# Performance work log

Hardware: AMD Instinct MI355X
Metric: run time of the kernel (lower is better)

Reference implementation:

```python
import jax, jax.numpy as jnp
import numpy as np

L, S, R, NUM_RESNET = 6, 2, 3, 3
N = 2 ** L            # 64 blocks per axis
NX = N * S            # 128 grid points per axis
NCART_SIDE = 80
NCART = NCART_SIDE ** 2


def _perm_idx(L_, l):
    delta = 2 ** (L_ - l - 1)
    t = np.tile(np.arange(2) * delta, delta) + np.repeat(np.arange(delta), 2)
    t = np.tile(t, 2 ** l) + np.repeat(np.arange(2 ** l) * 2 ** (L_ - l), 2 ** (L_ - l))
    return jnp.asarray(t)


def _switch_idx(L_):
    h = L_ // 2
    t = np.tile(np.arange(2 ** h) * 2 ** h, 2 ** h) + np.repeat(np.arange(2 ** h), 2 ** h)
    return jnp.asarray(t)


def _bmm2(x, g_left, g_right):
    # x: (B,p,i,q,j). Right block-diag GEMM on (q,j), then left block-diag GEMM on (p,i).
    y = jnp.einsum('bpiqj,qjk->bpiqk', x, g_right)
    return jnp.einsum('bpiqk,pio->bpoqk', y, g_left)


def _complex_layer(xr, xi, p):
    # p: stacked (r1,i1,r2,i2,r3,i3,r4,i4); complex-style cross products of the original.
    r1, i1, r2, i2, r3, i3, r4, i4 = p
    yr = _bmm2(xr, r1, r1) + _bmm2(xr, i1, i1) + _bmm2(xi, r2, i2) + _bmm2(xi, i2, r2)
    yi = _bmm2(xi, r3, r3) + _bmm2(xi, i3, i3) + _bmm2(xr, r4, i4) + _bmm2(xr, i4, r4)
    return yr, yi


def _u_layer(xr, xi, p):
    ur1, ui1, ur2, ui2, ur3, ui3, ur4, ui4 = p
    return (_bmm2(xr, ur1, ur1) + _bmm2(xr, ui2, ui2)
            + _bmm2(xi, ur3, ui3) + _bmm2(xi, ui4, ur4))


def _permute(yr, yi, idx):
    yr = jnp.take(jnp.take(yr, idx, axis=1), idx, axis=3)
    yi = jnp.take(jnp.take(yi, idx, axis=1), idx, axis=3)
    return yr, yi


def _merge(y):  # (B,N,R,N,R) -> (B,N/2,2R,N/2,2R)
    return y.reshape(y.shape[0], N // 2, 2 * R, N // 2, 2 * R)


def _split(y):  # inverse of _merge
    return y.reshape(y.shape[0], N, R, N, R)


def reference(x, Vp, Hp, Mp, Gp, Up, cart_mat, r_index):
    B = x.shape[0]
    xr = x[..., 0].reshape(B, N, S, N, S)
    xi = x[..., 1].reshape(B, N, S, N, S)
    yr, yi = _complex_layer(xr, xi, Vp)                       # (B,N,R,N,R)
    for li, l in enumerate(range(L - 1, L // 2 - 1, -1)):     # H stages (permute then merge-GEMM)
        yr, yi = _permute(yr, yi, _perm_idx(L, l))
        yr, yi = _complex_layer(_merge(yr), _merge(yi), Hp[li])
        yr, yi = _split(yr), _split(yi)
    yr, yi = _permute(yr, yi, _switch_idx(L))                 # middle switch shuffle
    for k in range(NUM_RESNET):                               # residual M blocks
        zr, zi = _complex_layer(yr, yi, Mp[k])
        yr, yi = yr + zr, yi + zi
    for li, l in enumerate(range(L // 2 - 1, -1, -1)):        # G stages (merge-GEMM then permute)
        yr, yi = _complex_layer(_merge(yr), _merge(yi), Gp[li])
        yr, yi = _split(yr), _split(yi)
        yr, yi = _permute(yr, yi, _perm_idx(L, l))
    y = _u_layer(yr, yi, Up).reshape(B, NX * NX)              # real output, (B,NX,NX) flattened
    y = jnp.take(y, r_index, axis=1)                          # polar reindexing
    out = y @ cart_mat.T                                      # polar -> cartesian interpolation
    return out.reshape(B, NCART_SIDE, NCART_SIDE)


def setup_inputs() -> dict:
    key = jax.random.key(0)
    ks = jax.random.split(key, 9)
    B = 128
    x = jax.random.normal(ks[0], (B, NX, NX, 2), dtype=jnp.float32)
    Vp = jax.random.normal(ks[1], (8, N, S, R), dtype=jnp.float32) * 0.35
    Hp = jax.random.normal(ks[2], (L // 2, 8, N // 2, 2 * R, 2 * R), dtype=jnp.float32) * 0.2
    Mp = jax.random.normal(ks[3], (NUM_RESNET, 8, N, R, R), dtype=jnp.float32) * 0.25
    Gp = jax.random.normal(ks[4], (L // 2, 8, N // 2, 2 * R, 2 * R), dtype=jnp.float32) * 0.2
    Up = jax.random.normal(ks[5], (8, N, R, S), dtype=jnp.float32) * 0.35
    cart_mat = jax.random.normal(ks[6], (NCART, NX * NX), dtype=jnp.float32) * 0.01
    r_index = jax.random.permutation(ks[7], NX * NX).astype(jnp.int32)
    return {"x": x, "Vp": Vp, "Hp": Hp, "Mp": Mp, "Gp": Gp, "Up": Up,
            "cart_mat": cart_mat, "r_index": r_index}
```

## Files before the change

kernel.cpp:

```cpp
#include <hip/hip_runtime.h>


typedef __attribute__((ext_vector_type(8))) short sx8;
typedef __attribute__((ext_vector_type(4))) float fx4;
typedef __attribute__((ext_vector_type(8))) unsigned short usx8;
typedef __attribute__((ext_vector_type(4))) unsigned short usx4;

__device__ __forceinline__ unsigned short f2bf(float f) {
  unsigned u = __builtin_bit_cast(unsigned, f);
  u = (u + 0x7FFFu + ((u >> 16) & 1u)) >> 16;
  return (unsigned short)u;
}

template<int ID>
__device__ __forceinline__ int rp_apply(int k) {
  if constexpr (ID == 0) { return k; }
  else if constexpr (ID == 3) { return (k & 7) * 8 + (k >> 3); }
  else {
    constexpr int l = (ID == 1) ? 4 : (ID == 2) ? 3 : (ID == 4) ? 2 : (ID == 5) ? 1 : 0;
    constexpr int d = 1 << (5 - l);
    constexpr int m2 = 2 * d;
    int g = k / m2, r = k % m2;
    return g * m2 + (r & 1) * d + (r >> 1);
  }
}

__global__ __launch_bounds__(256) void k_transpose(const float* __restrict__ x,
                                                   float* __restrict__ xtr,
                                                   float* __restrict__ xti) {
  __shared__ float ls[2][32][129];
  const int t = threadIdx.x;
  const int u = blockIdx.x;
  const int v0 = blockIdx.y * 32;
  for (int it = 0; it < 32; ++it) {
    int b = it * 4 + (t >> 6);
    int r = t & 63;
    int v = r >> 1, ch = r & 1;
    ls[ch][v][b] = x[(((size_t)b * 128 + u) * 128 + (v0 + v)) * 2 + ch];
  }
  __syncthreads();
  for (int it = 0; it < 32; ++it) {
    int idx = it * 256 + t;
    int ch = idx >> 12;
    int v = (idx >> 7) & 31;
    int b = idx & 127;
    float* dst = ch ? xti : xtr;
    dst[((size_t)(u * 128 + v0 + v)) * 128 + b] = ls[ch][v][b];
  }
}

__global__ __launch_bounds__(128) void k_v(const float* __restrict__ xtr,
                                           const float* __restrict__ xti,
                                           float* __restrict__ yr,
                                           float* __restrict__ yi,
                                           const float* __restrict__ wp) {
  const int b = threadIdx.x;
  const int p = blockIdx.x, q = blockIdx.y;
  float X[4], Yr[9], Yi[9];
#pragma unroll
  for (int k = 0; k < 9; ++k) { Yr[k] = 0.f; Yi[k] = 0.f; }

  auto loadX = [&](const float* src) {
#pragma unroll
    for (int i = 0; i < 2; ++i)
#pragma unroll
      for (int j = 0; j < 2; ++j)
        X[i * 2 + j] = src[((size_t)((2 * p + i) * 128 + (2 * q + j))) * 128 + b];
  };
  auto term = [&](float* Y, int lm, int rm) {
    const float* Lw = wp + ((size_t)lm * 64 + p) * 6;
    const float* Rw = wp + ((size_t)rm * 64 + q) * 6;
#pragma unroll
    for (int i = 0; i < 2; ++i) {
      float t0 = X[i*2+0] * Rw[0] + X[i*2+1] * Rw[3];
      float t1 = X[i*2+0] * Rw[1] + X[i*2+1] * Rw[4];
      float t2 = X[i*2+0] * Rw[2] + X[i*2+1] * Rw[5];
#pragma unroll
      for (int o = 0; o < 3; ++o) {
        float lv = Lw[i * 3 + o];
        Y[o*3+0] += lv * t0; Y[o*3+1] += lv * t1; Y[o*3+2] += lv * t2;
      }
    }
  };
  loadX(xtr);
  term(Yr, 0, 0); term(Yr, 1, 1); term(Yi, 6, 7); term(Yi, 7, 6);
  loadX(xti);
  term(Yr, 2, 3); term(Yr, 3, 2); term(Yi, 4, 4); term(Yi, 5, 5);
#pragma unroll
  for (int o = 0; o < 3; ++o)
#pragma unroll
    for (int k = 0; k < 3; ++k) {
      size_t off = ((size_t)((p * 3 + o) * 192 + (q * 3 + k))) * 128 + b;
      yr[off] = Yr[o * 3 + k];
      yi[off] = Yi[o * 3 + k];
    }
}

template<int PERM>
__global__ __launch_bounds__(128) void k_hg(const float* __restrict__ xr,
                                            const float* __restrict__ xi,
                                            float* __restrict__ yr,
                                            float* __restrict__ yi,
                                            const float* __restrict__ wp) {
  const int b = threadIdx.x;
  const int P = blockIdx.x, Q = blockIdx.y;
  int rrow[6], rcol[6];
#pragma unroll
  for (int I = 0; I < 6; ++I) {
    rrow[I] = rp_apply<PERM>(2 * P + I / 3) * 3 + I % 3;
    rcol[I] = rp_apply<PERM>(2 * Q + I / 3) * 3 + I % 3;
  }
  float X[36], Yr[36], Yi[36];
#pragma unroll
  for (int k = 0; k < 36; ++k) { Yr[k] = 0.f; Yi[k] = 0.f; }

  auto loadX = [&](const float* src) {
#pragma unroll
    for (int I = 0; I < 6; ++I)
#pragma unroll
      for (int J = 0; J < 6; ++J)
        X[I * 6 + J] = src[((size_t)(rrow[I] * 192 + rcol[J])) * 128 + b];
  };
  auto term = [&](float* Y, int lm, int rm) {
    const float* Lw = wp + ((size_t)lm * 32 + P) * 36;
    const float* Rw = wp + ((size_t)rm * 32 + Q) * 36;
#pragma unroll
    for (int i = 0; i < 6; ++i) {
      float tk[6];
#pragma unroll
      for (int k = 0; k < 6; ++k) tk[k] = 0.f;
#pragma unroll
      for (int j = 0; j < 6; ++j) {
        float xv = X[i * 6 + j];
#pragma unroll
        for (int k = 0; k < 6; ++k) tk[k] += xv * Rw[j * 6 + k];
      }
#pragma unroll
      for (int o = 0; o < 6; ++o) {
        float lv = Lw[i * 6 + o];
#pragma unroll
        for (int k = 0; k < 6; ++k) Y[o * 6 + k] += lv * tk[k];
      }
    }
  };
  loadX(xr);
  term(Yr, 0, 0); term(Yr, 1, 1); term(Yi, 6, 7); term(Yi, 7, 6);
  loadX(xi);
  term(Yr, 2, 3); term(Yr, 3, 2); term(Yi, 4, 4); term(Yi, 5, 5);
#pragma unroll
  for (int I = 0; I < 6; ++I)
#pragma unroll
    for (int J = 0; J < 6; ++J) {
      size_t off = ((size_t)((P * 6 + I) * 192 + (Q * 6 + J))) * 128 + b;
      yr[off] = Yr[I * 6 + J];
      yi[off] = Yi[I * 6 + J];
    }
}

template<int PERM>
__global__ __launch_bounds__(128) void k_m(const float* __restrict__ xr,
                                           const float* __restrict__ xi,
                                           float* __restrict__ yr,
                                           float* __restrict__ yi,
                                           const float* __restrict__ wp) {
  const int b = threadIdx.x;
  const int p = blockIdx.x, q = blockIdx.y;
  int rrow[3], rcol[3];
#pragma unroll
  for (int i = 0; i < 3; ++i) {
    rrow[i] = rp_apply<PERM>(p) * 3 + i;
    rcol[i] = rp_apply<PERM>(q) * 3 + i;
  }
  float X[9], Yr[9], Yi[9];
  auto loadX = [&](const float* src) {
#pragma unroll
    for (int i = 0; i < 3; ++i)
#pragma unroll
      for (int j = 0; j < 3; ++j)
        X[i * 3 + j] = src[((size_t)(rrow[i] * 192 + rcol[j])) * 128 + b];
  };
  auto term = [&](float* Y, int lm, int rm) {
    const float* Lw = wp + ((size_t)lm * 64 + p) * 9;
    const float* Rw = wp + ((size_t)rm * 64 + q) * 9;
#pragma unroll
    for (int i = 0; i < 3; ++i) {
      float t0 = X[i*3+0] * Rw[0] + X[i*3+1] * Rw[3] + X[i*3+2] * Rw[6];
      float t1 = X[i*3+0] * Rw[1] + X[i*3+1] * Rw[4] + X[i*3+2] * Rw[7];
      float t2 = X[i*3+0] * Rw[2] + X[i*3+1] * Rw[5] + X[i*3+2] * Rw[8];
#pragma unroll
      for (int o = 0; o < 3; ++o) {
        float lv = Lw[i * 3 + o];
        Y[o*3+0] += lv * t0; Y[o*3+1] += lv * t1; Y[o*3+2] += lv * t2;
      }
    }
  };
  loadX(xr);
#pragma unroll
  for (int k = 0; k < 9; ++k) { Yr[k] = X[k]; Yi[k] = 0.f; }
  term(Yr, 0, 0); term(Yr, 1, 1); term(Yi, 6, 7); term(Yi, 7, 6);
  loadX(xi);
#pragma unroll
  for (int k = 0; k < 9; ++k) Yi[k] += X[k];
  term(Yr, 2, 3); term(Yr, 3, 2); term(Yi, 4, 4); term(Yi, 5, 5);
#pragma unroll
  for (int o = 0; o < 3; ++o)
#pragma unroll
    for (int k = 0; k < 3; ++k) {
      size_t off = ((size_t)((p * 3 + o) * 192 + (q * 3 + k))) * 128 + b;
      yr[off] = Yr[o * 3 + k];
      yi[off] = Yi[o * 3 + k];
    }
}

__global__ __launch_bounds__(128) void k_u(const float* __restrict__ xr,
                                           const float* __restrict__ xi,
                                           float* __restrict__ ut,
                                           const float* __restrict__ wp) {
  const int b = threadIdx.x;
  const int p = blockIdx.x, q = blockIdx.y;
  int rrow[3], rcol[3];
#pragma unroll
  for (int i = 0; i < 3; ++i) {
    rrow[i] = rp_apply<6>(p) * 3 + i;
    rcol[i] = rp_apply<6>(q) * 3 + i;
  }
  float X[9], Y[4] = {0.f, 0.f, 0.f, 0.f};
  auto loadX = [&](const float* src) {
#pragma unroll
    for (int i = 0; i < 3; ++i)
#pragma unroll
      for (int j = 0; j < 3; ++j)
        X[i * 3 + j] = src[((size_t)(rrow[i] * 192 + rcol[j])) * 128 + b];
  };
  auto term = [&](int lm, int rm) {
    const float* Lw = wp + ((size_t)lm * 64 + p) * 6;
    const float* Rw = wp + ((size_t)rm * 64 + q) * 6;
#pragma unroll
    for (int i = 0; i < 3; ++i) {
      float t0 = X[i*3+0] * Rw[0] + X[i*3+1] * Rw[2] + X[i*3+2] * Rw[4];
      float t1 = X[i*3+0] * Rw[1] + X[i*3+1] * Rw[3] + X[i*3+2] * Rw[5];
      Y[0] += Lw[i*2+0] * t0; Y[1] += Lw[i*2+0] * t1;
      Y[2] += Lw[i*2+1] * t0; Y[3] += Lw[i*2+1] * t1;
    }
  };
  loadX(xr); term(0, 0); term(3, 3);
  loadX(xi); term(4, 5); term(7, 6);
#pragma unroll
  for (int o = 0; o < 2; ++o)
#pragma unroll
    for (int k = 0; k < 2; ++k)
      ut[((size_t)((p * 2 + o) * 128 + (q * 2 + k))) * 128 + b] = Y[o * 2 + k];
}

__global__ __launch_bounds__(256) void k_gather(const float* __restrict__ ut,
                                                const int* __restrict__ r_index,
                                                unsigned short* __restrict__ yg) {
  __shared__ float ls[64][129];
  __shared__ int ridx[64];
  const int t = threadIdx.x;
  const int m0 = blockIdx.x * 64;
  if (t < 64) ridx[t] = r_index[m0 + t];
  __syncthreads();
  for (int it = 0; it < 32; ++it) {
    int idx = it * 256 + t;
    int ml = idx >> 7, b = idx & 127;
    ls[ml][b] = ut[(size_t)ridx[ml] * 128 + b];
  }
  __syncthreads();
  int b = t >> 1, half = t & 1;
#pragma unroll
  for (int c = 0; c < 4; ++c) {
    usx8 v;
#pragma unroll
    for (int e = 0; e < 8; ++e) v[e] = f2bf(ls[half * 32 + c * 8 + e][b]);
    *(usx8*)(yg + (size_t)b * 16384 + m0 + half * 32 + c * 8) = v;
  }
}

#define GEMM_KC 16
#define GEMM_NKS 32

__global__ __launch_bounds__(256) void k_gemm(const unsigned short* __restrict__ yg,
                                              const float* __restrict__ cart,
                                              float* __restrict__ partial) {
  __shared__ unsigned short As[2][128][40];
  __shared__ unsigned short Bs[2][128][40];
  const int t = threadIdx.x;
  const int lane = t & 63, w = t >> 6;
  const int wm = w >> 1, wn = w & 1;
  const int c0 = blockIdx.x * 128;
  const int k0 = blockIdx.y * 1024;
  const int kc = blockIdx.y;

  fx4 acc[4][4];
#pragma unroll
  for (int i = 0; i < 4; ++i)
#pragma unroll
    for (int j = 0; j < 4; ++j) acc[i][j] = (fx4)0.f;

  auto ldA = [&](int rep, int kpos) -> usx8 {
    int c = t + rep * 256;
    return *(const usx8*)(yg + (size_t)(c >> 2) * 16384 + kpos + (c & 3) * 8);
  };
  auto stA = [&](int buf, int rep, usx8 v) {
    int c = t + rep * 256;
    *(usx8*)(&As[buf][c >> 2][(c & 3) * 8]) = v;
  };
  auto ldB = [&](int rep, int kpos) -> fx4 {
    int c = t + rep * 256;
    return *(const fx4*)(cart + (size_t)(c0 + (c >> 3)) * 16384 + kpos + (c & 7) * 4);
  };
  auto stB = [&](int buf, int rep, fx4 f) {
    int c = t + rep * 256;
    usx4 v;
    v[0] = f2bf(f[0]); v[1] = f2bf(f[1]); v[2] = f2bf(f[2]); v[3] = f2bf(f[3]);
    *(usx4*)(&Bs[buf][c >> 3][(c & 7) * 4]) = v;
  };

  {
    usx8 a0 = ldA(0, k0), a1 = ldA(1, k0);
    fx4 b0 = ldB(0, k0), b1 = ldB(1, k0), b2 = ldB(2, k0), b3 = ldB(3, k0);
    stA(0, 0, a0); stA(0, 1, a1);
    stB(0, 0, b0); stB(0, 1, b1); stB(0, 2, b2); stB(0, 3, b3);
  }
  __syncthreads();

  for (int s = 0; s < GEMM_NKS; ++s) {
    const int cur = s & 1;
    usx8 av0, av1; fx4 bv0, bv1, bv2, bv3;
    const bool pf = (s + 1 < GEMM_NKS);
    if (pf) {
      int kpos = k0 + (s + 1) * 32;
      av0 = ldA(0, kpos); av1 = ldA(1, kpos);
      bv0 = ldB(0, kpos); bv1 = ldB(1, kpos); bv2 = ldB(2, kpos); bv3 = ldB(3, kpos);
    }
    sx8 af[4], bfr[4];
#pragma unroll
    for (int mi = 0; mi < 4; ++mi) {
      int row = wm * 64 + mi * 16 + (lane & 15);
      af[mi] = *(const sx8*)(&As[cur][row][(lane >> 4) * 8]);
    }
#pragma unroll
    for (int ni = 0; ni < 4; ++ni) {
      int row = wn * 64 + ni * 16 + (lane & 15);
      bfr[ni] = *(const sx8*)(&Bs[cur][row][(lane >> 4) * 8]);
    }
#pragma unroll
    for (int mi = 0; mi < 4; ++mi)
#pragma unroll
      for (int ni = 0; ni < 4; ++ni)
        acc[mi][ni] = __builtin_amdgcn_mfma_f32_16x16x32_bf16(af[mi], bfr[ni], acc[mi][ni], 0, 0, 0);
    if (pf) {
      stA(cur ^ 1, 0, av0); stA(cur ^ 1, 1, av1);
      stB(cur ^ 1, 0, bv0); stB(cur ^ 1, 1, bv1); stB(cur ^ 1, 2, bv2); stB(cur ^ 1, 3, bv3);
    }
    __syncthreads();
  }

#pragma unroll
  for (int mi = 0; mi < 4; ++mi) {
    int brow = wm * 64 + mi * 16 + (lane >> 4) * 4;
#pragma unroll
    for (int ni = 0; ni < 4; ++ni) {
      int cc = c0 + wn * 64 + ni * 16 + (lane & 15);
#pragma unroll
      for (int r = 0; r < 4; ++r)
        partial[((size_t)kc * 128 + brow + r) * 6400 + cc] = acc[mi][ni][r];
    }
  }
}

__global__ __launch_bounds__(256) void k_reduce(const float* __restrict__ partial,
                                                float* __restrict__ out) {
  int i = blockIdx.x * 256 + threadIdx.x;
  fx4 s = (fx4)0.f;
#pragma unroll
  for (int kc = 0; kc < GEMM_KC; ++kc)
    s += *(const fx4*)(partial + (size_t)kc * 819200 + (size_t)i * 4);
  *(fx4*)(out + (size_t)i * 4) = s;
}

extern "C" void kernel_launch(void* const* d_in, const int* in_sizes, int n_in,
                              void* d_out, int out_size, void* d_ws, size_t ws_size,
                              hipStream_t stream) {
  const float* x    = (const float*)d_in[0];
  const float* Vp   = (const float*)d_in[1];
  const float* Hp   = (const float*)d_in[2];
  const float* Mp   = (const float*)d_in[3];
  const float* Gp   = (const float*)d_in[4];
  const float* Up   = (const float*)d_in[5];
  const float* cart = (const float*)d_in[6];
  const int*   ridx = (const int*)d_in[7];
  float* out = (float*)d_out;
  float* ws  = (float*)d_ws;

  const size_t PSZ = 4718592;
  float* P0r = ws;
  float* P0i = ws + PSZ;
  float* P1r = ws + 2 * PSZ;
  float* P1i = ws + 3 * PSZ;
  float* xtr = ws + 4 * PSZ;
  float* xti = xtr + 2097152;
  float* ut  = ws + 4 * PSZ;
  unsigned short* yg = (unsigned short*)(ws + 4 * PSZ + 2097152);
  float* partial = ws;

  const size_t HSZ = 8 * 32 * 36;
  const size_t MSZ = 8 * 64 * 9;

  k_transpose<<<dim3(128, 4), 256, 0, stream>>>(x, xtr, xti);
  k_v<<<dim3(64, 64), 128, 0, stream>>>(xtr, xti, P0r, P0i, Vp);
  k_hg<0><<<dim3(32, 32), 128, 0, stream>>>(P0r, P0i, P1r, P1i, Hp + 0 * HSZ);
  k_hg<1><<<dim3(32, 32), 128, 0, stream>>>(P1r, P1i, P0r, P0i, Hp + 1 * HSZ);
  k_hg<2><<<dim3(32, 32), 128, 0, stream>>>(P0r, P0i, P1r, P1i, Hp + 2 * HSZ);
  k_m<3><<<dim3(64, 64), 128, 0, stream>>>(P1r, P1i, P0r, P0i, Mp + 0 * MSZ);
  k_m<0><<<dim3(64, 64), 128, 0, stream>>>(P0r, P0i, P1r, P1i, Mp + 1 * MSZ);
  k_m<0><<<dim3(64, 64), 128, 0, stream>>>(P1r, P1i, P0r, P0i, Mp + 2 * MSZ);
  k_hg<0><<<dim3(32, 32), 128, 0, stream>>>(P0r, P0i, P1r, P1i, Gp + 0 * HSZ);
  k_hg<4><<<dim3(32, 32), 128, 0, stream>>>(P1r, P1i, P0r, P0i, Gp + 1 * HSZ);
  k_hg<5><<<dim3(32, 32), 128, 0, stream>>>(P0r, P0i, P1r, P1i, Gp + 2 * HSZ);
  k_u<<<dim3(64, 64), 128, 0, stream>>>(P1r, P1i, ut, Up);
  k_gather<<<dim3(256), 256, 0, stream>>>(ut, ridx, yg);
  k_gemm<<<dim3(50, GEMM_KC), 256, 0, stream>>>(yg, cart, partial);
  k_reduce<<<dim3(800), 256, 0, stream>>>(partial, out);
  (void)in_sizes; (void)n_in; (void)out_size; (void)ws_size;
}
```

Baseline: 346.3 us.

## Fuse V with first H stage, fuse M stages with first G stage, bf16 intermediates

Merges the V layer into the first H-stage kernel and the three M resnet layers plus the first G stage into one kernel, so each thread computes a 2x2 group of small blocks in registers before applying the 6x6 merge GEMM. This removes four launches and several full read/write passes of the large intermediate buffers. The U output and the GEMM split-K partials are also stored as bf16 instead of fp32, halving that traffic at some cost in precision. The fused kernels keep many more live registers, which may lower occupancy or cause spills.

```diff
diff --git a/kernel.cpp b/kernel.cpp
--- a/kernel.cpp
+++ b/kernel.cpp
@@ -10,6 +10,9 @@
   unsigned u = __builtin_bit_cast(unsigned, f);
   u = (u + 0x7FFFu + ((u >> 16) & 1u)) >> 16;
   return (unsigned short)u;
+}
+__device__ __forceinline__ float bf2f(unsigned short h) {
+  return __builtin_bit_cast(float, ((unsigned)h) << 16);
 }
 
 template<int ID>
@@ -49,50 +52,94 @@
   }
 }
 
-__global__ __launch_bounds__(128) void k_v(const float* __restrict__ xtr,
-                                           const float* __restrict__ xti,
-                                           float* __restrict__ yr,
-                                           float* __restrict__ yi,
-                                           const float* __restrict__ wp) {
+__global__ __launch_bounds__(128) void k_vh(const float* __restrict__ xtr,
+                                            const float* __restrict__ xti,
+                                            float* __restrict__ yr,
+                                            float* __restrict__ yi,
+                                            const float* __restrict__ vp,
+                                            const float* __restrict__ hp) {
   const int b = threadIdx.x;
-  const int p = blockIdx.x, q = blockIdx.y;
-  float X[4], Yr[9], Yi[9];
-#pragma unroll
-  for (int k = 0; k < 9; ++k) { Yr[k] = 0.f; Yi[k] = 0.f; }
-
-  auto loadX = [&](const float* src) {
-#pragma unroll
-    for (int i = 0; i < 2; ++i)
-#pragma unroll
-      for (int j = 0; j < 2; ++j)
-        X[i * 2 + j] = src[((size_t)((2 * p + i) * 128 + (2 * q + j))) * 128 + b];
-  };
-  auto term = [&](float* Y, int lm, int rm) {
-    const float* Lw = wp + ((size_t)lm * 64 + p) * 6;
-    const float* Rw = wp + ((size_t)rm * 64 + q) * 6;
-#pragma unroll
-    for (int i = 0; i < 2; ++i) {
-      float t0 = X[i*2+0] * Rw[0] + X[i*2+1] * Rw[3];
-      float t1 = X[i*2+0] * Rw[1] + X[i*2+1] * Rw[4];
-      float t2 = X[i*2+0] * Rw[2] + X[i*2+1] * Rw[5];
-#pragma unroll
-      for (int o = 0; o < 3; ++o) {
-        float lv = Lw[i * 3 + o];
-        Y[o*3+0] += lv * t0; Y[o*3+1] += lv * t1; Y[o*3+2] += lv * t2;
-      }
-    }
-  };
-  loadX(xtr);
-  term(Yr, 0, 0); term(Yr, 1, 1); term(Yi, 6, 7); term(Yi, 7, 6);
-  loadX(xti);
-  term(Yr, 2, 3); term(Yr, 3, 2); term(Yi, 4, 4); term(Yi, 5, 5);
-#pragma unroll
-  for (int o = 0; o < 3; ++o)
-#pragma unroll
-    for (int k = 0; k < 3; ++k) {
-      size_t off = ((size_t)((p * 3 + o) * 192 + (q * 3 + k))) * 128 + b;
-      yr[off] = Yr[o * 3 + k];
-      yi[off] = Yi[o * 3 + k];
+  const int P = blockIdx.x, Q = blockIdx.y;
+  float Vr[36], Vi[36];
+
+#pragma unroll
+  for (int pp = 0; pp < 2; ++pp)
+#pragma unroll
+    for (int qq = 0; qq < 2; ++qq) {
+      const int p = 2 * P + pp, q = 2 * Q + qq;
+      float Xr[4], Xi[4];
+#pragma unroll
+      for (int i = 0; i < 2; ++i)
+#pragma unroll
+        for (int j = 0; j < 2; ++j) {
+          size_t off = ((size_t)((4 * P + 2 * pp + i) * 128 + (4 * Q + 2 * qq + j))) * 128 + b;
+          Xr[i * 2 + j] = xtr[off];
+          Xi[i * 2 + j] = xti[off];
+        }
+      float Ar[9], Ai[9];
+#pragma unroll
+      for (int k = 0; k < 9; ++k) { Ar[k] = 0.f; Ai[k] = 0.f; }
+      auto termV = [&](float* Y, const float* X, int lm, int rm) {
+        const float* Lw = vp + ((size_t)lm * 64 + p) * 6;
+        const float* Rw = vp + ((size_t)rm * 64 + q) * 6;
+#pragma unroll
+        for (int i = 0; i < 2; ++i) {
+          float t0 = X[i*2+0] * Rw[0] + X[i*2+1] * Rw[3];
+          float t1 = X[i*2+0] * Rw[1] + X[i*2+1] * Rw[4];
+          float t2 = X[i*2+0] * Rw[2] + X[i*2+1] * Rw[5];
+#pragma unroll
+          for (int o = 0; o < 3; ++o) {
+            float lv = Lw[i * 3 + o];
+            Y[o*3+0] += lv * t0; Y[o*3+1] += lv * t1; Y[o*3+2] += lv * t2;
+          }
+        }
+      };
+      termV(Ar, Xr, 0, 0); termV(Ar, Xr, 1, 1); termV(Ai, Xr, 6, 7); termV(Ai, Xr, 7, 6);
+      termV(Ar, Xi, 2, 3); termV(Ar, Xi, 3, 2); termV(Ai, Xi, 4, 4); termV(Ai, Xi, 5, 5);
+#pragma unroll
+      for (int o = 0; o < 3; ++o)
+#pragma unroll
+        for (int k = 0; k < 3; ++k) {
+          Vr[(3 * pp + o) * 6 + 3 * qq + k] = Ar[o * 3 + k];
+          Vi[(3 * pp + o) * 6 + 3 * qq + k] = Ai[o * 3 + k];
+        }
+    }
+
+  float Yr[36], Yi[36];
+#pragma unroll
+  for (int k = 0; k < 36; ++k) { Yr[k] = 0.f; Yi[k] = 0.f; }
+  auto termH = [&](float* Y, const float* X, int lm, int rm) {
+    const float* Lw = hp + ((size_t)lm * 32 + P) * 36;
+    const float* Rw = hp + ((size_t)rm * 32 + Q) * 36;
+#pragma unroll
+    for (int i = 0; i < 6; ++i) {
+      float tk[6];
+#pragma unroll
+      for (int k = 0; k < 6; ++k) tk[k] = 0.f;
+#pragma unroll
+      for (int j = 0; j < 6; ++j) {
+        float xv = X[i * 6 + j];
+#pragma unroll
+        for (int k = 0; k < 6; ++k) tk[k] += xv * Rw[j * 6 + k];
+      }
+#pragma unroll
+      for (int o = 0; o < 6; ++o) {
+        float lv = Lw[i * 6 + o];
+#pragma unroll
+        for (int k = 0; k < 6; ++k) Y[o * 6 + k] += lv * tk[k];
+      }
+    }
+  };
+  termH(Yr, Vr, 0, 0); termH(Yr, Vr, 1, 1); termH(Yi, Vr, 6, 7); termH(Yi, Vr, 7, 6);
+  termH(Yr, Vi, 2, 3); termH(Yr, Vi, 3, 2); termH(Yi, Vi, 4, 4); termH(Yi, Vi, 5, 5);
+
+#pragma unroll
+  for (int I = 0; I < 6; ++I)
+#pragma unroll
+    for (int J = 0; J < 6; ++J) {
+      size_t off = ((size_t)((P * 6 + I) * 192 + (Q * 6 + J))) * 128 + b;
+      yr[off] = Yr[I * 6 + J];
+      yi[off] = Yi[I * 6 + J];
     }
 }
 
@@ -157,64 +204,107 @@
     }
 }
 
-template<int PERM>
-__global__ __launch_bounds__(128) void k_m(const float* __restrict__ xr,
-                                           const float* __restrict__ xi,
-                                           float* __restrict__ yr,
-                                           float* __restrict__ yi,
-                                           const float* __restrict__ wp) {
+__global__ __launch_bounds__(128) void k_mg(const float* __restrict__ xr,
+                                            const float* __restrict__ xi,
+                                            float* __restrict__ yr,
+                                            float* __restrict__ yi,
+                                            const float* __restrict__ mp,
+                                            const float* __restrict__ gp) {
   const int b = threadIdx.x;
-  const int p = blockIdx.x, q = blockIdx.y;
-  int rrow[3], rcol[3];
-#pragma unroll
-  for (int i = 0; i < 3; ++i) {
-    rrow[i] = rp_apply<PERM>(p) * 3 + i;
-    rcol[i] = rp_apply<PERM>(q) * 3 + i;
-  }
-  float X[9], Yr[9], Yi[9];
-  auto loadX = [&](const float* src) {
-#pragma unroll
-    for (int i = 0; i < 3; ++i)
-#pragma unroll
-      for (int j = 0; j < 3; ++j)
-        X[i * 3 + j] = src[((size_t)(rrow[i] * 192 + rcol[j])) * 128 + b];
-  };
-  auto term = [&](float* Y, int lm, int rm) {
-    const float* Lw = wp + ((size_t)lm * 64 + p) * 9;
-    const float* Rw = wp + ((size_t)rm * 64 + q) * 9;
-#pragma unroll
-    for (int i = 0; i < 3; ++i) {
-      float t0 = X[i*3+0] * Rw[0] + X[i*3+1] * Rw[3] + X[i*3+2] * Rw[6];
-      float t1 = X[i*3+0] * Rw[1] + X[i*3+1] * Rw[4] + X[i*3+2] * Rw[7];
-      float t2 = X[i*3+0] * Rw[2] + X[i*3+1] * Rw[5] + X[i*3+2] * Rw[8];
-#pragma unroll
-      for (int o = 0; o < 3; ++o) {
-        float lv = Lw[i * 3 + o];
-        Y[o*3+0] += lv * t0; Y[o*3+1] += lv * t1; Y[o*3+2] += lv * t2;
-      }
-    }
-  };
-  loadX(xr);
-#pragma unroll
-  for (int k = 0; k < 9; ++k) { Yr[k] = X[k]; Yi[k] = 0.f; }
-  term(Yr, 0, 0); term(Yr, 1, 1); term(Yi, 6, 7); term(Yi, 7, 6);
-  loadX(xi);
-#pragma unroll
-  for (int k = 0; k < 9; ++k) Yi[k] += X[k];
-  term(Yr, 2, 3); term(Yr, 3, 2); term(Yi, 4, 4); term(Yi, 5, 5);
-#pragma unroll
-  for (int o = 0; o < 3; ++o)
-#pragma unroll
-    for (int k = 0; k < 3; ++k) {
-      size_t off = ((size_t)((p * 3 + o) * 192 + (q * 3 + k))) * 128 + b;
-      yr[off] = Yr[o * 3 + k];
-      yi[off] = Yi[o * 3 + k];
+  const int P = blockIdx.x, Q = blockIdx.y;
+  float Vr[36], Vi[36];
+
+#pragma unroll
+  for (int aa = 0; aa < 2; ++aa)
+#pragma unroll
+    for (int bb = 0; bb < 2; ++bb) {
+      const int p = 2 * P + aa, q = 2 * Q + bb;
+      const int prow = rp_apply<3>(p) * 3, pcol = rp_apply<3>(q) * 3;
+      float Xr[9], Xi[9];
+#pragma unroll
+      for (int i = 0; i < 3; ++i)
+#pragma unroll
+        for (int j = 0; j < 3; ++j) {
+          size_t off = ((size_t)((prow + i) * 192 + (pcol + j))) * 128 + b;
+          Xr[i * 3 + j] = xr[off];
+          Xi[i * 3 + j] = xi[off];
+        }
+#pragma unroll
+      for (int lk = 0; lk < 3; ++lk) {
+        const float* wp = mp + (size_t)lk * (8 * 64 * 9);
+        float Yr9[9], Yi9[9];
+#pragma unroll
+        for (int k = 0; k < 9; ++k) { Yr9[k] = Xr[k]; Yi9[k] = Xi[k]; }
+        auto termM = [&](float* Y, const float* X, int lm, int rm) {
+          const float* Lw = wp + ((size_t)lm * 64 + p) * 9;
+          const float* Rw = wp + ((size_t)rm * 64 + q) * 9;
+#pragma unroll
+          for (int i = 0; i < 3; ++i) {
+            float t0 = X[i*3+0] * Rw[0] + X[i*3+1] * Rw[3] + X[i*3+2] * Rw[6];
+            float t1 = X[i*3+0] * Rw[1] + X[i*3+1] * Rw[4] + X[i*3+2] * Rw[7];
+            float t2 = X[i*3+0] * Rw[2] + X[i*3+1] * Rw[5] + X[i*3+2] * Rw[8];
+#pragma unroll
+            for (int o = 0; o < 3; ++o) {
+              float lv = Lw[i * 3 + o];
+              Y[o*3+0] += lv * t0; Y[o*3+1] += lv * t1; Y[o*3+2] += lv * t2;
+            }
+          }
+        };
+        termM(Yr9, Xr, 0, 0); termM(Yr9, Xr, 1, 1); termM(Yi9, Xr, 6, 7); termM(Yi9, Xr, 7, 6);
+        termM(Yr9, Xi, 2, 3); termM(Yr9, Xi, 3, 2); termM(Yi9, Xi, 4, 4); termM(Yi9, Xi, 5, 5);
+#pragma unroll
+        for (int k = 0; k < 9; ++k) { Xr[k] = Yr9[k]; Xi[k] = Yi9[k]; }
+      }
+#pragma unroll
+      for (int i = 0; i < 3; ++i)
+#pragma unroll
+        for (int j = 0; j < 3; ++j) {
+          Vr[(3 * aa + i) * 6 + 3 * bb + j] = Xr[i * 3 + j];
+          Vi[(3 * aa + i) * 6 + 3 * bb + j] = Xi[i * 3 + j];
+        }
+    }
+
+  float Yr[36], Yi[36];
+#pragma unroll
+  for (int k = 0; k < 36; ++k) { Yr[k] = 0.f; Yi[k] = 0.f; }
+  auto termH = [&](float* Y, const float* X, int lm, int rm) {
+    const float* Lw = gp + ((size_t)lm * 32 + P) * 36;
+    const float* Rw = gp + ((size_t)rm * 32 + Q) * 36;
+#pragma unroll
+    for (int i = 0; i < 6; ++i) {
+      float tk[6];
+#pragma unroll
+      for (int k = 0; k < 6; ++k) tk[k] = 0.f;
+#pragma unroll
+      for (int j = 0; j < 6; ++j) {
+        float xv = X[i * 6 + j];
+#pragma unroll
+        for (int k = 0; k < 6; ++k) tk[k] += xv * Rw[j * 6 + k];
+      }
+#pragma unroll
+      for (int o = 0; o < 6; ++o) {
+        float lv = Lw[i * 6 + o];
+#pragma unroll
+        for (int k = 0; k < 6; ++k) Y[o * 6 + k] += lv * tk[k];
+      }
+    }
+  };
+  termH(Yr, Vr, 0, 0); termH(Yr, Vr, 1, 1); termH(Yi, Vr, 6, 7); termH(Yi, Vr, 7, 6);
+  termH(Yr, Vi, 2, 3); termH(Yr, Vi, 3, 2); termH(Yi, Vi, 4, 4); termH(Yi, Vi, 5, 5);
+
+#pragma unroll
+  for (int I = 0; I < 6; ++I)
+#pragma unroll
+    for (int J = 0; J < 6; ++J) {
+      size_t off = ((size_t)((P * 6 + I) * 192 + (Q * 6 + J))) * 128 + b;
+      yr[off] = Yr[I * 6 + J];
+      yi[off] = Yi[I * 6 + J];
     }
 }
 
 __global__ __launch_bounds__(128) void k_u(const float* __restrict__ xr,
                                            const float* __restrict__ xi,
-                                           float* __restrict__ ut,
+                                           unsigned short* __restrict__ ut,
                                            const float* __restrict__ wp) {
   const int b = threadIdx.x;
   const int p = blockIdx.x, q = blockIdx.y;
@@ -249,13 +339,13 @@
   for (int o = 0; o < 2; ++o)
 #pragma unroll
     for (int k = 0; k < 2; ++k)
-      ut[((size_t)((p * 2 + o) * 128 + (q * 2 + k))) * 128 + b] = Y[o * 2 + k];
-}
-
-__global__ __launch_bounds__(256) void k_gather(const float* __restrict__ ut,
+      ut[((size_t)((p * 2 + o) * 128 + (q * 2 + k))) * 128 + b] = f2bf(Y[o * 2 + k]);
+}
+
+__global__ __launch_bounds__(256) void k_gather(const unsigned short* __restrict__ ut,
                                                 const int* __restrict__ r_index,
                                                 unsigned short* __restrict__ yg) {
-  __shared__ float ls[64][129];
+  __shared__ unsigned short ls[64][130];
   __shared__ int ridx[64];
   const int t = threadIdx.x;
   const int m0 = blockIdx.x * 64;
@@ -272,7 +362,7 @@
   for (int c = 0; c < 4; ++c) {
     usx8 v;
 #pragma unroll
-    for (int e = 0; e < 8; ++e) v[e] = f2bf(ls[half * 32 + c * 8 + e][b]);
+    for (int e = 0; e < 8; ++e) v[e] = ls[half * 32 + c * 8 + e][b];
     *(usx8*)(yg + (size_t)b * 16384 + m0 + half * 32 + c * 8) = v;
   }
 }
@@ -282,7 +372,7 @@
 
 __global__ __launch_bounds__(256) void k_gemm(const unsigned short* __restrict__ yg,
                                               const float* __restrict__ cart,
-                                              float* __restrict__ partial) {
+                                              unsigned short* __restrict__ partial) {
   __shared__ unsigned short As[2][128][40];
   __shared__ unsigned short Bs[2][128][40];
   const int t = threadIdx.x;
@@ -365,18 +455,20 @@
       int cc = c0 + wn * 64 + ni * 16 + (lane & 15);
 #pragma unroll
       for (int r = 0; r < 4; ++r)
-        partial[((size_t)kc * 128 + brow + r) * 6400 + cc] = acc[mi][ni][r];
-    }
-  }
-}
-
-__global__ __launch_bounds__(256) void k_reduce(const float* __restrict__ partial,
+        partial[((size_t)kc * 128 + brow + r) * 6400 + cc] = f2bf(acc[mi][ni][r]);
+    }
+  }
+}
+
+__global__ __launch_bounds__(256) void k_reduce(const unsigned short* __restrict__ partial,
                                                 float* __restrict__ out) {
   int i = blockIdx.x * 256 + threadIdx.x;
   fx4 s = (fx4)0.f;
 #pragma unroll
-  for (int kc = 0; kc < GEMM_KC; ++kc)
-    s += *(const fx4*)(partial + (size_t)kc * 819200 + (size_t)i * 4);
+  for (int kc = 0; kc < GEMM_KC; ++kc) {
+    usx4 v = *(const usx4*)(partial + (size_t)kc * 819200 + (size_t)i * 4);
+    s[0] += bf2f(v[0]); s[1] += bf2f(v[1]); s[2] += bf2f(v[2]); s[3] += bf2f(v[3]);
+  }
   *(fx4*)(out + (size_t)i * 4) = s;
 }
 
@@ -401,22 +493,17 @@
   float* P1i = ws + 3 * PSZ;
   float* xtr = ws + 4 * PSZ;
   float* xti = xtr + 2097152;
-  float* ut  = ws + 4 * PSZ;
-  unsigned short* yg = (unsigned short*)(ws + 4 * PSZ + 2097152);
-  float* partial = ws;
+  unsigned short* ut = (unsigned short*)(ws + 4 * PSZ);
+  unsigned short* yg = (unsigned short*)(ws + 4 * PSZ + 1048576);
+  unsigned short* partial = (unsigned short*)ws;
 
   const size_t HSZ = 8 * 32 * 36;
-  const size_t MSZ = 8 * 64 * 9;
 
   k_transpose<<<dim3(128, 4), 256, 0, stream>>>(x, xtr, xti);
-  k_v<<<dim3(64, 64), 128, 0, stream>>>(xtr, xti, P0r, P0i, Vp);
-  k_hg<0><<<dim3(32, 32), 128, 0, stream>>>(P0r, P0i, P1r, P1i, Hp + 0 * HSZ);
-  k_hg<1><<<dim3(32, 32), 128, 0, stream>>>(P1r, P1i, P0r, P0i, Hp + 1 * HSZ);
-  k_hg<2><<<dim3(32, 32), 128, 0, stream>>>(P0r, P0i, P1r, P1i, Hp + 2 * HSZ);
-  k_m<3><<<dim3(64, 64), 128, 0, stream>>>(P1r, P1i, P0r, P0i, Mp + 0 * MSZ);
-  k_m<0><<<dim3(64, 64), 128, 0, stream>>>(P0r, P0i, P1r, P1i, Mp + 1 * MSZ);
-  k_m<0><<<dim3(64, 64), 128, 0, stream>>>(P1r, P1i, P0r, P0i, Mp + 2 * MSZ);
-  k_hg<0><<<dim3(32, 32), 128, 0, stream>>>(P0r, P0i, P1r, P1i, Gp + 0 * HSZ);
+  k_vh<<<dim3(32, 32), 128, 0, stream>>>(xtr, xti, P0r, P0i, Vp, Hp + 0 * HSZ);
+  k_hg<1><<<dim3(32, 32), 128, 0, stream>>>(P0r, P0i, P1r, P1i, Hp + 1 * HSZ);
+  k_hg<2><<<dim3(32, 32), 128, 0, stream>>>(P1r, P1i, P0r, P0i, Hp + 2 * HSZ);
+  k_mg<<<dim3(32, 32), 128, 0, stream>>>(P0r, P0i, P1r, P1i, Mp, Gp + 0 * HSZ);
   k_hg<4><<<dim3(32, 32), 128, 0, stream>>>(P1r, P1i, P0r, P0i, Gp + 1 * HSZ);
   k_hg<5><<<dim3(32, 32), 128, 0, stream>>>(P0r, P0i, P1r, P1i, Gp + 2 * HSZ);
   k_u<<<dim3(64, 64), 128, 0, stream>>>(P1r, P1i, ut, Up);
```

Result: slower. 360.4 us (+4.1%).
